# Performance work log

Hardware: AMD Instinct MI355X
Metric: run time of the kernel (lower is better)

The kernel has to match this reference:

```python
import jax, jax.numpy as jnp
import numpy as np

DIM = 128
LAYERS = 3
N_NODES = 50000
N_EDGES = 640000
LN_EPS = 1e-5


def setup_inputs() -> dict:
    key = jax.random.key(0)
    ks = jax.random.split(key, 10)
    s = 1.0 / np.sqrt(DIM)
    x = jax.random.normal(ks[0], (N_NODES, DIM), dtype=jnp.float32)
    edge_index = jax.random.randint(ks[1], (2, N_EDGES), 0, N_NODES, dtype=jnp.int64)
    in_w = jax.random.uniform(ks[2], (DIM, DIM), jnp.float32, -s, s)
    in_b = jax.random.uniform(ks[3], (DIM,), jnp.float32, -s, s)
    w1 = jax.random.uniform(ks[4], (LAYERS, DIM, DIM), jnp.float32, -s, s)
    b1 = jax.random.uniform(ks[5], (LAYERS, DIM), jnp.float32, -s, s)
    w2 = jax.random.uniform(ks[6], (LAYERS, DIM, DIM), jnp.float32, -s, s)
    b2 = jax.random.uniform(ks[7], (LAYERS, DIM), jnp.float32, -s, s)
    ln_g = jnp.ones((LAYERS, DIM), jnp.float32)
    ln_b = jnp.zeros((LAYERS, DIM), jnp.float32)
    return {"x": x, "edge_index": edge_index, "in_w": in_w, "in_b": in_b,
            "w1": w1, "b1": b1, "w2": w2, "b2": b2, "ln_g": ln_g, "ln_b": ln_b}


def _layer_norm(z, g, b):
    mu = jnp.mean(z, axis=-1, keepdims=True)
    var = jnp.mean(jnp.square(z - mu), axis=-1, keepdims=True)
    return (z - mu) * jax.lax.rsqrt(var + LN_EPS) * g + b


def reference(x, edge_index, in_w, in_b, w1, b1, w2, b2, ln_g, ln_b):
    src, dst = edge_index[0], edge_index[1]
    n = x.shape[0]
    # degree is identical every layer in the original; compute once (same math)
    deg = jax.ops.segment_sum(jnp.ones(dst.shape, x.dtype), dst, num_segments=n)
    deg = jnp.maximum(deg, 1.0)[:, None]  # [N,1]
    h = x @ in_w + in_b  # [N,D]
    for i in range(w1.shape[0]):
        m = jax.ops.segment_sum(h[src], dst, num_segments=n) / deg  # gather+scatter
        mlp = jax.nn.relu(m @ w1[i] + b1[i]) @ w2[i] + b2[i]
        h = _layer_norm(h + mlp, ln_g[i], ln_b[i])
    return h
```

## Files before the change

### kernel.cpp

```cpp
#include <hip/hip_runtime.h>
#include <hip/hip_fp8.h>

#define DIM 128
#define LN_EPS 1e-5f

typedef __attribute__((ext_vector_type(8))) short s16x8;
typedef __attribute__((ext_vector_type(4))) float f32x4;
typedef __attribute__((ext_vector_type(2))) float f32x2;
typedef __attribute__((ext_vector_type(4))) unsigned int u32x4;

__device__ __forceinline__ unsigned short f2bf(float f) {
    unsigned u = __float_as_uint(f);
    unsigned r = u + 0x7fffu + ((u >> 16) & 1u);
    return (unsigned short)(r >> 16);
}
__device__ __forceinline__ float bf2f(unsigned short b) {
    return __uint_as_float(((unsigned)b) << 16);
}
__device__ __forceinline__ unsigned char f2fp8(float f) {
    return (unsigned char)__hip_cvt_float_to_fp8(f, __HIP_SATFINITE, __HIP_E4M3);
}
__device__ __forceinline__ void acc_fp8x4(float* a, unsigned v) {
    f32x2 lo = __builtin_amdgcn_cvt_pk_f32_fp8(v, false);
    f32x2 hi = __builtin_amdgcn_cvt_pk_f32_fp8(v, true);
    a[0] += lo[0]; a[1] += lo[1]; a[2] += hi[0]; a[3] += hi[1];
}
__device__ __forceinline__ void acc_fp8x16(float* a, u32x4 v) {
    acc_fp8x4(a + 0,  v[0]);
    acc_fp8x4(a + 4,  v[1]);
    acc_fp8x4(a + 8,  v[2]);
    acc_fp8x4(a + 12, v[3]);
}


__global__ __launch_bounds__(256) void prep(const float* __restrict__ in_w,
                                            const float* __restrict__ w1,
                                            const float* __restrict__ w2,
                                            unsigned short* __restrict__ wt, int L,
                                            const int* __restrict__ dst, int E,
                                            int* __restrict__ counts, int nWblk) {
    if ((int)blockIdx.x < nWblk) {
        int mat = blockIdx.x >> 3, part = blockIdx.x & 7;
        const float* src;
        if (mat == 0) src = in_w;
        else if (mat <= L) src = w1 + (size_t)(mat - 1) * DIM * DIM;
        else src = w2 + (size_t)(mat - 1 - L) * DIM * DIM;
        unsigned short* dstw = wt + (size_t)mat * DIM * DIM;
        int base = part * 2048 + threadIdx.x;
#pragma unroll
        for (int j = 0; j < 8; ++j) {
            int i = base + j * 256;
            int k = i >> 7, n = i & 127;
            dstw[n * DIM + k] = f2bf(src[i]);
        }
    } else {
        int b = blockIdx.x - nWblk;
        int i = (b * 256 + threadIdx.x) * 4;
        if (i + 3 < E) {
            int4 d = *(const int4*)(dst + i);
            atomicAdd(&counts[d.x], 1);
            atomicAdd(&counts[d.y], 1);
            atomicAdd(&counts[d.z], 1);
            atomicAdd(&counts[d.w], 1);
        } else {
            for (int j = i; j < E; ++j) atomicAdd(&counts[dst[j]], 1);
        }
    }
}


__global__ __launch_bounds__(256) void scan_all(const int* __restrict__ counts, int n,
                                                int* __restrict__ rowptr,
                                                int* __restrict__ cursor,
                                                float* __restrict__ dinv, int E) {
    __shared__ int wsum[4];
    int tid = threadIdx.x;
    int lane = tid & 63, wid = tid >> 6;

    int limit = blockIdx.x * 1024;
    int acc = 0;
    for (int i = tid * 4; i < limit; i += 1024) {
        int4 c4 = *(const int4*)(counts + i);
        acc += c4.x + c4.y + c4.z + c4.w;
    }
#pragma unroll
    for (int off = 32; off > 0; off >>= 1) acc += __shfl_xor(acc, off, 64);
    if (lane == 0) wsum[wid] = acc;
    __syncthreads();
    int bofs = wsum[0] + wsum[1] + wsum[2] + wsum[3];
    __syncthreads();

    if (blockIdx.x == 0 && tid == 0) rowptr[n] = E;

    int base = blockIdx.x * 1024 + tid * 4;
    int v[4];
#pragma unroll
    for (int j = 0; j < 4; ++j) {
        int i = base + j;
        v[j] = (i < n) ? counts[i] : 0;
    }
    int tsum = v[0] + v[1] + v[2] + v[3];
    int incl = tsum;
#pragma unroll
    for (int off = 1; off < 64; off <<= 1) {
        int t = __shfl_up(incl, off, 64);
        if (lane >= off) incl += t;
    }
    if (lane == 63) wsum[wid] = incl;
    __syncthreads();
    int wofs = 0;
    for (int w = 0; w < 4; ++w)
        if (w < wid) wofs += wsum[w];
    int excl = bofs + wofs + (incl - tsum);
#pragma unroll
    for (int j = 0; j < 4; ++j) {
        int i = base + j;
        if (i < n) {
            rowptr[i] = excl;
            cursor[i] = excl;
            dinv[i] = 1.0f / (float)((v[j] > 1) ? v[j] : 1);
            excl += v[j];
        }
    }
}


__global__ void fill_csr(const int* __restrict__ src, const int* __restrict__ dst, int E,
                         int* __restrict__ cursor, unsigned short* __restrict__ srcidx) {
    int i = (blockIdx.x * 256 + threadIdx.x) * 4;
    if (i + 3 < E) {
        int4 s4 = *(const int4*)(src + i);
        int4 d4 = *(const int4*)(dst + i);
        int p0 = atomicAdd(&cursor[d4.x], 1); srcidx[p0] = (unsigned short)s4.x;
        int p1 = atomicAdd(&cursor[d4.y], 1); srcidx[p1] = (unsigned short)s4.y;
        int p2 = atomicAdd(&cursor[d4.z], 1); srcidx[p2] = (unsigned short)s4.z;
        int p3 = atomicAdd(&cursor[d4.w], 1); srcidx[p3] = (unsigned short)s4.w;
    } else {
        for (int j = i; j < E; ++j) {
            int p = atomicAdd(&cursor[dst[j]], 1);
            srcidx[p] = (unsigned short)src[j];
        }
    }
}


__global__ __launch_bounds__(256) void gemm_bias32(const float* __restrict__ x,
                                                   const unsigned short* __restrict__ Wt,
                                                   const float* __restrict__ bias,
                                                   unsigned short* __restrict__ hb,
                                                   unsigned char* __restrict__ h8, int N) {
    __shared__ __align__(16) unsigned short X[32][136];
    __shared__ __align__(16) float Z[32][132];
    __shared__ __align__(16) float bias_s[128];

    int tid = threadIdx.x;
    int w = tid >> 6, lane = tid & 63;
    int quad = lane >> 4, l16 = lane & 15;
    int r0 = blockIdx.x * 32;
    int cs = w * 32;

    if (tid < 32) *(float4*)(bias_s + tid * 4) = *(const float4*)(bias + tid * 4);

    {
        int row = tid >> 3;
        int c0 = (tid & 7) * 16;
        int grow = r0 + row;
        u32x4 o0 = {0, 0, 0, 0}, o1 = {0, 0, 0, 0};
        if (grow < N) {
            const float4* xp = (const float4*)(x + ((size_t)grow << 7) + c0);
            float4 f0 = xp[0], f1 = xp[1], f2 = xp[2], f3 = xp[3];
            o0[0] = (unsigned)f2bf(f0.x) | ((unsigned)f2bf(f0.y) << 16);
            o0[1] = (unsigned)f2bf(f0.z) | ((unsigned)f2bf(f0.w) << 16);
            o0[2] = (unsigned)f2bf(f1.x) | ((unsigned)f2bf(f1.y) << 16);
            o0[3] = (unsigned)f2bf(f1.z) | ((unsigned)f2bf(f1.w) << 16);
            o1[0] = (unsigned)f2bf(f2.x) | ((unsigned)f2bf(f2.y) << 16);
            o1[1] = (unsigned)f2bf(f2.z) | ((unsigned)f2bf(f2.w) << 16);
            o1[2] = (unsigned)f2bf(f3.x) | ((unsigned)f2bf(f3.y) << 16);
            o1[3] = (unsigned)f2bf(f3.z) | ((unsigned)f2bf(f3.w) << 16);
        }
        *(u32x4*)(&X[row][c0])     = o0;
        *(u32x4*)(&X[row][c0 + 8]) = o1;
    }
    __syncthreads();

    f32x4 ac[2][2];
    ac[0][0] = (f32x4){0.f, 0.f, 0.f, 0.f}; ac[0][1] = (f32x4){0.f, 0.f, 0.f, 0.f};
    ac[1][0] = (f32x4){0.f, 0.f, 0.f, 0.f}; ac[1][1] = (f32x4){0.f, 0.f, 0.f, 0.f};
#pragma unroll
    for (int k0 = 0; k0 < 128; k0 += 32) {
        s16x8 b0 = *(const s16x8*)(Wt + ((size_t)(cs + l16) << 7) + quad * 8 + k0);
        s16x8 b1 = *(const s16x8*)(Wt + ((size_t)(cs + 16 + l16) << 7) + quad * 8 + k0);
        s16x8 a0 = *(const s16x8*)(&X[l16][quad * 8 + k0]);
        s16x8 a1 = *(const s16x8*)(&X[16 + l16][quad * 8 + k0]);
        ac[0][0] = __builtin_amdgcn_mfma_f32_16x16x32_bf16(a0, b0, ac[0][0], 0, 0, 0);
        ac[0][1] = __builtin_amdgcn_mfma_f32_16x16x32_bf16(a0, b1, ac[0][1], 0, 0, 0);
        ac[1][0] = __builtin_amdgcn_mfma_f32_16x16x32_bf16(a1, b0, ac[1][0], 0, 0, 0);
        ac[1][1] = __builtin_amdgcn_mfma_f32_16x16x32_bf16(a1, b1, ac[1][1], 0, 0, 0);
    }

#pragma unroll
    for (int rt = 0; rt < 2; ++rt) {
#pragma unroll
        for (int c = 0; c < 2; ++c) {
            int col = cs + c * 16 + l16;
            float bv = bias_s[col];
#pragma unroll
            for (int reg = 0; reg < 4; ++reg) {
                Z[rt * 16 + quad * 4 + reg][col] = ac[rt][c][reg] + bv;
            }
        }
    }
    __syncthreads();

    {
        int row = tid >> 3;
        int c0 = (tid & 7) * 16;
        int grow = r0 + row;
        if (grow < N) {
            u32x4 ob0, ob1, o8;
#pragma unroll
            for (int j = 0; j < 4; ++j) {
                float v0 = Z[row][c0 + 2 * j];
                float v1 = Z[row][c0 + 2 * j + 1];
                float v2 = Z[row][c0 + 8 + 2 * j];
                float v3 = Z[row][c0 + 8 + 2 * j + 1];
                ob0[j] = (unsigned)f2bf(v0) | ((unsigned)f2bf(v1) << 16);
                ob1[j] = (unsigned)f2bf(v2) | ((unsigned)f2bf(v3) << 16);
                float w0 = Z[row][c0 + 4 * j], w1 = Z[row][c0 + 4 * j + 1];
                float w2 = Z[row][c0 + 4 * j + 2], w3 = Z[row][c0 + 4 * j + 3];
                o8[j] = (unsigned)f2fp8(w0) | ((unsigned)f2fp8(w1) << 8)
                      | ((unsigned)f2fp8(w2) << 16) | ((unsigned)f2fp8(w3) << 24);
            }
            *(u32x4*)(hb + ((size_t)grow << 7) + c0)     = ob0;
            *(u32x4*)(hb + ((size_t)grow << 7) + c0 + 8) = ob1;
            *(u32x4*)(h8 + ((size_t)grow << 7) + c0)     = o8;
        }
    }
}


__global__ __launch_bounds__(256) void aggregate(const unsigned char* __restrict__ h8in,
                                                 const int* __restrict__ rowptr,
                                                 const unsigned short* __restrict__ srcidx,
                                                 const float* __restrict__ dinv,
                                                 unsigned short* __restrict__ mout, int N) {
    int tid = threadIdx.x;
    int w = tid >> 6, lane = tid & 63;
    int g = lane >> 3, li = lane & 7;
    int nd = blockIdx.x * 32 + w * 8 + g;
    bool nv = nd < N;

    int e  = nv ? rowptr[nd] : 0;
    int ee = nv ? rowptr[nd + 1] : 0;
    float di = nv ? dinv[nd] : 0.f;

    const unsigned char* hsl = h8in + li * 16;

    float a[16];
#pragma unroll
    for (int j = 0; j < 16; ++j) a[j] = 0.f;

#define GIDX(jj) (((jj) < ee) ? (int)srcidx[(jj)] : -1)
    int jA = e;
    int iA0 = GIDX(jA + 0), iA1 = GIDX(jA + 1), iA2 = GIDX(jA + 2), iA3 = GIDX(jA + 3);
    u32x4 A0 = {0, 0, 0, 0}, A1 = {0, 0, 0, 0}, A2 = {0, 0, 0, 0}, A3 = {0, 0, 0, 0};
    if (iA0 >= 0) A0 = *(const u32x4*)(hsl + ((size_t)iA0 << 7));
    if (iA1 >= 0) A1 = *(const u32x4*)(hsl + ((size_t)iA1 << 7));
    if (iA2 >= 0) A2 = *(const u32x4*)(hsl + ((size_t)iA2 << 7));
    if (iA3 >= 0) A3 = *(const u32x4*)(hsl + ((size_t)iA3 << 7));
    int jB = jA + 4;
    int iB0 = GIDX(jB + 0), iB1 = GIDX(jB + 1), iB2 = GIDX(jB + 2), iB3 = GIDX(jB + 3);

    while (__any(jA < ee)) {
        u32x4 B0 = {0, 0, 0, 0}, B1v = {0, 0, 0, 0}, B2v = {0, 0, 0, 0}, B3 = {0, 0, 0, 0};
        if (iB0 >= 0) B0  = *(const u32x4*)(hsl + ((size_t)iB0 << 7));
        if (iB1 >= 0) B1v = *(const u32x4*)(hsl + ((size_t)iB1 << 7));
        if (iB2 >= 0) B2v = *(const u32x4*)(hsl + ((size_t)iB2 << 7));
        if (iB3 >= 0) B3  = *(const u32x4*)(hsl + ((size_t)iB3 << 7));
        int jC = jB + 4;
        int iC0 = GIDX(jC + 0), iC1 = GIDX(jC + 1), iC2 = GIDX(jC + 2), iC3 = GIDX(jC + 3);
        acc_fp8x16(a, A0);
        acc_fp8x16(a, A1);
        acc_fp8x16(a, A2);
        acc_fp8x16(a, A3);
        jA = jB; A0 = B0; A1 = B1v; A2 = B2v; A3 = B3;
        jB = jC; iB0 = iC0; iB1 = iC1; iB2 = iC2; iB3 = iC3;
    }
#undef GIDX

    if (nv) {
        u32x4 o0, o1;
#pragma unroll
        for (int j = 0; j < 4; ++j) {
            unsigned lo0 = f2bf(a[2 * j]     * di);
            unsigned hi0 = f2bf(a[2 * j + 1] * di);
            o0[j] = lo0 | (hi0 << 16);
            unsigned lo1 = f2bf(a[8 + 2 * j]     * di);
            unsigned hi1 = f2bf(a[8 + 2 * j + 1] * di);
            o1[j] = lo1 | (hi1 << 16);
        }
        unsigned short* mp = mout + ((size_t)nd << 7) + li * 16;
        *(u32x4*)(mp)     = o0;
        *(u32x4*)(mp + 8) = o1;
    }
}


__global__ __launch_bounds__(256) void mlp_ln(const unsigned short* __restrict__ hin,
                                              const unsigned short* __restrict__ m,
                                              const unsigned short* __restrict__ W1t,
                                              const float* __restrict__ B1,
                                              const unsigned short* __restrict__ W2t,
                                              const float* __restrict__ B2,
                                              const float* __restrict__ G,
                                              const float* __restrict__ Bb,
                                              unsigned short* __restrict__ hout,
                                              unsigned char* __restrict__ h8out,
                                              float* __restrict__ out_f32, int N) {
    __shared__ unsigned short M[32][132];
    __shared__ unsigned short P[32][132];
    __shared__ float s1p[4][32], s2p[4][32];

    int tid = threadIdx.x;
    int w = tid >> 6, lane = tid & 63;
    int quad = lane >> 4, l16 = lane & 15;
    int r0 = blockIdx.x * 32;
    int cs = w * 32;

#pragma unroll
    for (int cc = 0; cc < 2; ++cc) {
        int c = tid + cc * 256;
        int row = c >> 4, colc = (c & 15) * 8;
        int grow = r0 + row;
        u32x4 v = {0, 0, 0, 0};
        if (grow < N) v = *(const u32x4*)(m + ((size_t)grow << 7) + colc);
        *(u32x4*)(&M[row][colc]) = v;
    }
    __syncthreads();

    unsigned short hvr[2][2][4];
#pragma unroll
    for (int rt = 0; rt < 2; ++rt) {
#pragma unroll
        for (int c = 0; c < 2; ++c) {
            int col = cs + c * 16 + l16;
#pragma unroll
            for (int reg = 0; reg < 4; ++reg) {
                int grow = r0 + rt * 16 + quad * 4 + reg;
                hvr[rt][c][reg] = (grow < N) ? hin[((size_t)grow << 7) + col] : (unsigned short)0;
            }
        }
    }

    f32x4 ac1[2][2];
    ac1[0][0] = (f32x4){0.f, 0.f, 0.f, 0.f}; ac1[0][1] = (f32x4){0.f, 0.f, 0.f, 0.f};
    ac1[1][0] = (f32x4){0.f, 0.f, 0.f, 0.f}; ac1[1][1] = (f32x4){0.f, 0.f, 0.f, 0.f};
#pragma unroll
    for (int k0 = 0; k0 < 128; k0 += 32) {
        s16x8 b0 = *(const s16x8*)(W1t + ((size_t)(cs + l16) << 7) + quad * 8 + k0);
        s16x8 b1 = *(const s16x8*)(W1t + ((size_t)(cs + 16 + l16) << 7) + quad * 8 + k0);
        s16x8 a0 = *(const s16x8*)(&M[l16][quad * 8 + k0]);
        s16x8 a1 = *(const s16x8*)(&M[16 + l16][quad * 8 + k0]);
        ac1[0][0] = __builtin_amdgcn_mfma_f32_16x16x32_bf16(a0, b0, ac1[0][0], 0, 0, 0);
        ac1[0][1] = __builtin_amdgcn_mfma_f32_16x16x32_bf16(a0, b1, ac1[0][1], 0, 0, 0);
        ac1[1][0] = __builtin_amdgcn_mfma_f32_16x16x32_bf16(a1, b0, ac1[1][0], 0, 0, 0);
        ac1[1][1] = __builtin_amdgcn_mfma_f32_16x16x32_bf16(a1, b1, ac1[1][1], 0, 0, 0);
    }
#pragma unroll
    for (int rt = 0; rt < 2; ++rt) {
#pragma unroll
        for (int c = 0; c < 2; ++c) {
            int col = cs + c * 16 + l16;
            float bv = B1[col];
#pragma unroll
            for (int reg = 0; reg < 4; ++reg) {
                float v = fmaxf(ac1[rt][c][reg] + bv, 0.f);
                P[rt * 16 + quad * 4 + reg][col] = f2bf(v);
            }
        }
    }
    __syncthreads();

    f32x4 ac2[2][2];
    ac2[0][0] = (f32x4){0.f, 0.f, 0.f, 0.f}; ac2[0][1] = (f32x4){0.f, 0.f, 0.f, 0.f};
    ac2[1][0] = (f32x4){0.f, 0.f, 0.f, 0.f}; ac2[1][1] = (f32x4){0.f, 0.f, 0.f, 0.f};
#pragma unroll
    for (int k0 = 0; k0 < 128; k0 += 32) {
        s16x8 b0 = *(const s16x8*)(W2t + ((size_t)(cs + l16) << 7) + quad * 8 + k0);
        s16x8 b1 = *(const s16x8*)(W2t + ((size_t)(cs + 16 + l16) << 7) + quad * 8 + k0);
        s16x8 a0 = *(const s16x8*)(&P[l16][quad * 8 + k0]);
        s16x8 a1 = *(const s16x8*)(&P[16 + l16][quad * 8 + k0]);
        ac2[0][0] = __builtin_amdgcn_mfma_f32_16x16x32_bf16(a0, b0, ac2[0][0], 0, 0, 0);
        ac2[0][1] = __builtin_amdgcn_mfma_f32_16x16x32_bf16(a0, b1, ac2[0][1], 0, 0, 0);
        ac2[1][0] = __builtin_amdgcn_mfma_f32_16x16x32_bf16(a1, b0, ac2[1][0], 0, 0, 0);
        ac2[1][1] = __builtin_amdgcn_mfma_f32_16x16x32_bf16(a1, b1, ac2[1][1], 0, 0, 0);
    }

    float z[2][2][4];
    float ps1[2][4] = {{0, 0, 0, 0}, {0, 0, 0, 0}};
    float ps2[2][4] = {{0, 0, 0, 0}, {0, 0, 0, 0}};
#pragma unroll
    for (int rt = 0; rt < 2; ++rt) {
#pragma unroll
        for (int c = 0; c < 2; ++c) {
            int col = cs + c * 16 + l16;
            float b2v = B2[col];
#pragma unroll
            for (int reg = 0; reg < 4; ++reg) {
                float hv = bf2f(hvr[rt][c][reg]);
                float zz = ac2[rt][c][reg] + b2v + hv;
                z[rt][c][reg] = zz;
                ps1[rt][reg] += zz;
                ps2[rt][reg] += zz * zz;
            }
        }
    }
#pragma unroll
    for (int off = 1; off < 16; off <<= 1) {
#pragma unroll
        for (int rt = 0; rt < 2; ++rt) {
#pragma unroll
            for (int reg = 0; reg < 4; ++reg) {
                ps1[rt][reg] += __shfl_xor(ps1[rt][reg], off, 64);
                ps2[rt][reg] += __shfl_xor(ps2[rt][reg], off, 64);
            }
        }
    }
    if (l16 == 0) {
#pragma unroll
        for (int rt = 0; rt < 2; ++rt) {
#pragma unroll
            for (int reg = 0; reg < 4; ++reg) {
                s1p[w][rt * 16 + quad * 4 + reg] = ps1[rt][reg];
                s2p[w][rt * 16 + quad * 4 + reg] = ps2[rt][reg];
            }
        }
    }
    __syncthreads();

#pragma unroll
    for (int rt = 0; rt < 2; ++rt) {
#pragma unroll
        for (int reg = 0; reg < 4; ++reg) {
            int row = rt * 16 + quad * 4 + reg;
            float S1 = s1p[0][row] + s1p[1][row] + s1p[2][row] + s1p[3][row];
            float S2 = s2p[0][row] + s2p[1][row] + s2p[2][row] + s2p[3][row];
            float mean = S1 * (1.0f / 128.0f);
            float var = S2 * (1.0f / 128.0f) - mean * mean;
            float rs = rsqrtf(var + LN_EPS);
            int grow = r0 + row;
            if (grow < N) {
#pragma unroll
                for (int c = 0; c < 2; ++c) {
                    int col = cs + c * 16 + l16;
                    float o = (z[rt][c][reg] - mean) * rs * G[col] + Bb[col];
                    if (out_f32) {
                        out_f32[((size_t)grow << 7) + col] = o;
                    } else {
                        hout[((size_t)grow << 7) + col] = f2bf(o);
                        h8out[((size_t)grow << 7) + col] = f2fp8(o);
                    }
                }
            }
        }
    }
}


extern "C" void kernel_launch(void* const* d_in, const int* in_sizes, int n_in,
                              void* d_out, int out_size, void* d_ws, size_t ws_size,
                              hipStream_t stream) {
    const float* x    = (const float*)d_in[0];
    const int*   ei   = (const int*)d_in[1];
    const float* in_w = (const float*)d_in[2];
    const float* in_b = (const float*)d_in[3];
    const float* w1   = (const float*)d_in[4];
    const float* b1   = (const float*)d_in[5];
    const float* w2   = (const float*)d_in[6];
    const float* b2   = (const float*)d_in[7];
    const float* ln_g = (const float*)d_in[8];
    const float* ln_b = (const float*)d_in[9];

    const int N = in_sizes[0] / DIM;
    const int E = in_sizes[1] / 2;
    const int LAYERS = in_sizes[4] / (DIM * DIM);

    const int* e_src = ei;
    const int* e_dst = ei + E;

    char* ws = (char*)d_ws;
    unsigned short* hb0    = (unsigned short*)ws;  ws += (size_t)N * DIM * 2;
    unsigned short* hb1    = (unsigned short*)ws;  ws += (size_t)N * DIM * 2;
    unsigned char*  h8a    = (unsigned char*)ws;   ws += (size_t)N * DIM;
    unsigned char*  h8b    = (unsigned char*)ws;   ws += (size_t)N * DIM;
    int*            counts = (int*)ws;             ws += (size_t)N * 4;
    int*            rowptr = (int*)ws;             ws += (size_t)(N + 1) * 4;
    int*            cursor = (int*)ws;             ws += (size_t)N * 4;
    float*          dinv   = (float*)ws;           ws += (size_t)N * 4;
    unsigned short* srcidx = (unsigned short*)ws;  ws += (size_t)E * 2;
    unsigned short* wt     = (unsigned short*)ws;  ws += (size_t)(2 * LAYERS + 1) * DIM * DIM * 2;
    unsigned short* mbuf   = (unsigned short*)ws;  ws += (size_t)N * DIM * 2;

    const int nScanBlocks = (N + 1023) / 1024;
    const int nMat = 2 * LAYERS + 1;
    const int nWblk = nMat * 8;

    (void)hipMemsetAsync(counts, 0, (size_t)N * 4, stream);
    prep<<<nWblk + (E + 1023) / 1024, 256, 0, stream>>>(in_w, w1, w2, wt, LAYERS,
                                                        e_dst, E, counts, nWblk);
    scan_all<<<nScanBlocks, 256, 0, stream>>>(counts, N, rowptr, cursor, dinv, E);
    gemm_bias32<<<(N + 31) / 32, 256, 0, stream>>>(x, wt, in_b, hb0, h8a, N);
    fill_csr<<<(E + 1023) / 1024, 256, 0, stream>>>(e_src, e_dst, E, cursor, srcidx);

    const unsigned short* w1t = wt + (size_t)DIM * DIM;
    const unsigned short* w2t = wt + (size_t)(1 + LAYERS) * DIM * DIM;

    int tile_grid = (N + 31) / 32;
    unsigned short* hin  = hb0;  unsigned char* h8in  = h8a;
    unsigned short* hout = hb1;  unsigned char* h8out = h8b;
    for (int i = 0; i < LAYERS; ++i) {
        float* out = (i == LAYERS - 1) ? (float*)d_out : nullptr;
        aggregate<<<tile_grid, 256, 0, stream>>>(h8in, rowptr, srcidx, dinv, mbuf, N);
        mlp_ln<<<tile_grid, 256, 0, stream>>>(hin, mbuf,
                                              w1t + (size_t)i * DIM * DIM, b1 + (size_t)i * DIM,
                                              w2t + (size_t)i * DIM * DIM, b2 + (size_t)i * DIM,
                                              ln_g + (size_t)i * DIM, ln_b + (size_t)i * DIM,
                                              hout, h8out, out, N);
        unsigned short* t = hin; hin = hout; hout = t;
        unsigned char* t8 = h8in; h8in = h8out; h8out = t8;
    }
}
```

Before: 321.6 us.

## Restructure MLP+LayerNorm kernel so each wave owns 16 full rows

The fused MLP/LayerNorm kernel now gives each wave 16 complete rows across all 128 output columns, instead of splitting columns across waves over a shared 32-row tile. The A operand is read straight from global memory, the ReLU intermediate goes to a per-wave LDS slice, and LayerNorm statistics are reduced with shuffles only. This removes all block-level barriers and the cross-wave LDS reduction. In exchange each wave holds more accumulators (16 f32x4 tiles), raising register pressure, and the block tile grows to 64 rows, so the grid is halved.

```diff
diff --git a/kernel.cpp b/kernel.cpp
--- a/kernel.cpp
+++ b/kernel.cpp
@@ -317,149 +317,116 @@
                                               unsigned short* __restrict__ hout,
                                               unsigned char* __restrict__ h8out,
                                               float* __restrict__ out_f32, int N) {
-    __shared__ unsigned short M[32][132];
-    __shared__ unsigned short P[32][132];
-    __shared__ float s1p[4][32], s2p[4][32];
+    __shared__ __align__(16) unsigned short Pw[4][16][136];
 
     int tid = threadIdx.x;
     int w = tid >> 6, lane = tid & 63;
     int quad = lane >> 4, l16 = lane & 15;
-    int r0 = blockIdx.x * 32;
-    int cs = w * 32;
-
-#pragma unroll
-    for (int cc = 0; cc < 2; ++cc) {
-        int c = tid + cc * 256;
-        int row = c >> 4, colc = (c & 15) * 8;
-        int grow = r0 + row;
-        u32x4 v = {0, 0, 0, 0};
-        if (grow < N) v = *(const u32x4*)(m + ((size_t)grow << 7) + colc);
-        *(u32x4*)(&M[row][colc]) = v;
-    }
-    __syncthreads();
-
-    unsigned short hvr[2][2][4];
-#pragma unroll
-    for (int rt = 0; rt < 2; ++rt) {
-#pragma unroll
-        for (int c = 0; c < 2; ++c) {
-            int col = cs + c * 16 + l16;
+    int rw = blockIdx.x * 64 + w * 16;
+
+    f32x4 ac1[8];
+#pragma unroll
+    for (int t = 0; t < 8; ++t) ac1[t] = (f32x4){0.f, 0.f, 0.f, 0.f};
+    {
+        int arow = rw + l16;
+        bool av = arow < N;
+        const unsigned short* ap = m + ((size_t)(av ? arow : 0) << 7) + quad * 8;
+#pragma unroll
+        for (int ks = 0; ks < 4; ++ks) {
+            s16x8 a = {0, 0, 0, 0, 0, 0, 0, 0};
+            if (av) a = *(const s16x8*)(ap + ks * 32);
+#pragma unroll
+            for (int t = 0; t < 8; ++t) {
+                s16x8 b = *(const s16x8*)(W1t + ((size_t)(t * 16 + l16) << 7) + quad * 8 + ks * 32);
+                ac1[t] = __builtin_amdgcn_mfma_f32_16x16x32_bf16(a, b, ac1[t], 0, 0, 0);
+            }
+        }
+    }
+
+#pragma unroll
+    for (int t = 0; t < 8; ++t) {
+        float bv = B1[t * 16 + l16];
+#pragma unroll
+        for (int reg = 0; reg < 4; ++reg) {
+            float v = fmaxf(ac1[t][reg] + bv, 0.f);
+            Pw[w][quad * 4 + reg][t * 16 + l16] = f2bf(v);
+        }
+    }
+
+    f32x4 ac2[8];
+#pragma unroll
+    for (int t = 0; t < 8; ++t) ac2[t] = (f32x4){0.f, 0.f, 0.f, 0.f};
+#pragma unroll
+    for (int ks = 0; ks < 4; ++ks) {
+        s16x8 a = *(const s16x8*)(&Pw[w][l16][quad * 8 + ks * 32]);
+#pragma unroll
+        for (int t = 0; t < 8; ++t) {
+            s16x8 b = *(const s16x8*)(W2t + ((size_t)(t * 16 + l16) << 7) + quad * 8 + ks * 32);
+            ac2[t] = __builtin_amdgcn_mfma_f32_16x16x32_bf16(a, b, ac2[t], 0, 0, 0);
+        }
+    }
+
+    float b2v[8], gv[8], bbv[8];
+#pragma unroll
+    for (int t = 0; t < 8; ++t) {
+        b2v[t] = B2[t * 16 + l16];
+        gv[t]  = G[t * 16 + l16];
+        bbv[t] = Bb[t * 16 + l16];
+    }
+    unsigned short hvu[8][4];
+#pragma unroll
+    for (int reg = 0; reg < 4; ++reg) {
+        int gr = rw + quad * 4 + reg;
+        bool gvld = gr < N;
+        const unsigned short* hp = hin + ((size_t)(gvld ? gr : 0) << 7);
+#pragma unroll
+        for (int t = 0; t < 8; ++t) {
+            hvu[t][reg] = gvld ? hp[t * 16 + l16] : (unsigned short)0;
+        }
+    }
+
+    float ps1[4][4], ps2[4][4];
+#pragma unroll
+    for (int vw = 0; vw < 4; ++vw) {
+#pragma unroll
+        for (int reg = 0; reg < 4; ++reg) {
+            float z0 = ac2[2 * vw][reg] + b2v[2 * vw] + bf2f(hvu[2 * vw][reg]);
+            float z1 = ac2[2 * vw + 1][reg] + b2v[2 * vw + 1] + bf2f(hvu[2 * vw + 1][reg]);
+            ps1[vw][reg] = z0 + z1;
+            ps2[vw][reg] = z0 * z0 + z1 * z1;
+        }
+    }
+#pragma unroll
+    for (int off = 1; off < 16; off <<= 1) {
+#pragma unroll
+        for (int vw = 0; vw < 4; ++vw) {
 #pragma unroll
             for (int reg = 0; reg < 4; ++reg) {
-                int grow = r0 + rt * 16 + quad * 4 + reg;
-                hvr[rt][c][reg] = (grow < N) ? hin[((size_t)grow << 7) + col] : (unsigned short)0;
+                ps1[vw][reg] += __shfl_xor(ps1[vw][reg], off, 64);
+                ps2[vw][reg] += __shfl_xor(ps2[vw][reg], off, 64);
             }
         }
     }
 
-    f32x4 ac1[2][2];
-    ac1[0][0] = (f32x4){0.f, 0.f, 0.f, 0.f}; ac1[0][1] = (f32x4){0.f, 0.f, 0.f, 0.f};
-    ac1[1][0] = (f32x4){0.f, 0.f, 0.f, 0.f}; ac1[1][1] = (f32x4){0.f, 0.f, 0.f, 0.f};
-#pragma unroll
-    for (int k0 = 0; k0 < 128; k0 += 32) {
-        s16x8 b0 = *(const s16x8*)(W1t + ((size_t)(cs + l16) << 7) + quad * 8 + k0);
-        s16x8 b1 = *(const s16x8*)(W1t + ((size_t)(cs + 16 + l16) << 7) + quad * 8 + k0);
-        s16x8 a0 = *(const s16x8*)(&M[l16][quad * 8 + k0]);
-        s16x8 a1 = *(const s16x8*)(&M[16 + l16][quad * 8 + k0]);
-        ac1[0][0] = __builtin_amdgcn_mfma_f32_16x16x32_bf16(a0, b0, ac1[0][0], 0, 0, 0);
-        ac1[0][1] = __builtin_amdgcn_mfma_f32_16x16x32_bf16(a0, b1, ac1[0][1], 0, 0, 0);
-        ac1[1][0] = __builtin_amdgcn_mfma_f32_16x16x32_bf16(a1, b0, ac1[1][0], 0, 0, 0);
-        ac1[1][1] = __builtin_amdgcn_mfma_f32_16x16x32_bf16(a1, b1, ac1[1][1], 0, 0, 0);
-    }
-#pragma unroll
-    for (int rt = 0; rt < 2; ++rt) {
-#pragma unroll
-        for (int c = 0; c < 2; ++c) {
-            int col = cs + c * 16 + l16;
-            float bv = B1[col];
-#pragma unroll
-            for (int reg = 0; reg < 4; ++reg) {
-                float v = fmaxf(ac1[rt][c][reg] + bv, 0.f);
-                P[rt * 16 + quad * 4 + reg][col] = f2bf(v);
-            }
-        }
-    }
-    __syncthreads();
-
-    f32x4 ac2[2][2];
-    ac2[0][0] = (f32x4){0.f, 0.f, 0.f, 0.f}; ac2[0][1] = (f32x4){0.f, 0.f, 0.f, 0.f};
-    ac2[1][0] = (f32x4){0.f, 0.f, 0.f, 0.f}; ac2[1][1] = (f32x4){0.f, 0.f, 0.f, 0.f};
-#pragma unroll
-    for (int k0 = 0; k0 < 128; k0 += 32) {
-        s16x8 b0 = *(const s16x8*)(W2t + ((size_t)(cs + l16) << 7) + quad * 8 + k0);
-        s16x8 b1 = *(const s16x8*)(W2t + ((size_t)(cs + 16 + l16) << 7) + quad * 8 + k0);
-        s16x8 a0 = *(const s16x8*)(&P[l16][quad * 8 + k0]);
-        s16x8 a1 = *(const s16x8*)(&P[16 + l16][quad * 8 + k0]);
-        ac2[0][0] = __builtin_amdgcn_mfma_f32_16x16x32_bf16(a0, b0, ac2[0][0], 0, 0, 0);
-        ac2[0][1] = __builtin_amdgcn_mfma_f32_16x16x32_bf16(a0, b1, ac2[0][1], 0, 0, 0);
-        ac2[1][0] = __builtin_amdgcn_mfma_f32_16x16x32_bf16(a1, b0, ac2[1][0], 0, 0, 0);
-        ac2[1][1] = __builtin_amdgcn_mfma_f32_16x16x32_bf16(a1, b1, ac2[1][1], 0, 0, 0);
-    }
-
-    float z[2][2][4];
-    float ps1[2][4] = {{0, 0, 0, 0}, {0, 0, 0, 0}};
-    float ps2[2][4] = {{0, 0, 0, 0}, {0, 0, 0, 0}};
-#pragma unroll
-    for (int rt = 0; rt < 2; ++rt) {
-#pragma unroll
-        for (int c = 0; c < 2; ++c) {
-            int col = cs + c * 16 + l16;
-            float b2v = B2[col];
-#pragma unroll
-            for (int reg = 0; reg < 4; ++reg) {
-                float hv = bf2f(hvr[rt][c][reg]);
-                float zz = ac2[rt][c][reg] + b2v + hv;
-                z[rt][c][reg] = zz;
-                ps1[rt][reg] += zz;
-                ps2[rt][reg] += zz * zz;
-            }
-        }
-    }
-#pragma unroll
-    for (int off = 1; off < 16; off <<= 1) {
-#pragma unroll
-        for (int rt = 0; rt < 2; ++rt) {
-#pragma unroll
-            for (int reg = 0; reg < 4; ++reg) {
-                ps1[rt][reg] += __shfl_xor(ps1[rt][reg], off, 64);
-                ps2[rt][reg] += __shfl_xor(ps2[rt][reg], off, 64);
-            }
-        }
-    }
-    if (l16 == 0) {
-#pragma unroll
-        for (int rt = 0; rt < 2; ++rt) {
-#pragma unroll
-            for (int reg = 0; reg < 4; ++reg) {
-                s1p[w][rt * 16 + quad * 4 + reg] = ps1[rt][reg];
-                s2p[w][rt * 16 + quad * 4 + reg] = ps2[rt][reg];
-            }
-        }
-    }
-    __syncthreads();
-
-#pragma unroll
-    for (int rt = 0; rt < 2; ++rt) {
-#pragma unroll
-        for (int reg = 0; reg < 4; ++reg) {
-            int row = rt * 16 + quad * 4 + reg;
-            float S1 = s1p[0][row] + s1p[1][row] + s1p[2][row] + s1p[3][row];
-            float S2 = s2p[0][row] + s2p[1][row] + s2p[2][row] + s2p[3][row];
-            float mean = S1 * (1.0f / 128.0f);
-            float var = S2 * (1.0f / 128.0f) - mean * mean;
-            float rs = rsqrtf(var + LN_EPS);
-            int grow = r0 + row;
-            if (grow < N) {
-#pragma unroll
-                for (int c = 0; c < 2; ++c) {
-                    int col = cs + c * 16 + l16;
-                    float o = (z[rt][c][reg] - mean) * rs * G[col] + Bb[col];
-                    if (out_f32) {
-                        out_f32[((size_t)grow << 7) + col] = o;
-                    } else {
-                        hout[((size_t)grow << 7) + col] = f2bf(o);
-                        h8out[((size_t)grow << 7) + col] = f2fp8(o);
-                    }
+#pragma unroll
+    for (int reg = 0; reg < 4; ++reg) {
+        float S1 = ((ps1[0][reg] + ps1[1][reg]) + ps1[2][reg]) + ps1[3][reg];
+        float S2 = ((ps2[0][reg] + ps2[1][reg]) + ps2[2][reg]) + ps2[3][reg];
+        float mean = S1 * (1.0f / 128.0f);
+        float var = S2 * (1.0f / 128.0f) - mean * mean;
+        float rs = rsqrtf(var + LN_EPS);
+        int gr = rw + quad * 4 + reg;
+        if (gr < N) {
+#pragma unroll
+            for (int t = 0; t < 8; ++t) {
+                int col = t * 16 + l16;
+                float z = ac2[t][reg] + b2v[t] + bf2f(hvu[t][reg]);
+                float o = (z - mean) * rs * gv[t] + bbv[t];
+                if (out_f32) {
+                    out_f32[((size_t)gr << 7) + col] = o;
+                } else {
+                    hout[((size_t)gr << 7) + col] = f2bf(o);
+                    h8out[((size_t)gr << 7) + col] = f2fp8(o);
                 }
             }
         }
@@ -515,17 +482,18 @@
     const unsigned short* w1t = wt + (size_t)DIM * DIM;
     const unsigned short* w2t = wt + (size_t)(1 + LAYERS) * DIM * DIM;
 
-    int tile_grid = (N + 31) / 32;
+    int agg_grid = (N + 31) / 32;
+    int mlp_grid = (N + 63) / 64;
     unsigned short* hin  = hb0;  unsigned char* h8in  = h8a;
     unsigned short* hout = hb1;  unsigned char* h8out = h8b;
     for (int i = 0; i < LAYERS; ++i) {
         float* out = (i == LAYERS - 1) ? (float*)d_out : nullptr;
-        aggregate<<<tile_grid, 256, 0, stream>>>(h8in, rowptr, srcidx, dinv, mbuf, N);
-        mlp_ln<<<tile_grid, 256, 0, stream>>>(hin, mbuf,
-                                              w1t + (size_t)i * DIM * DIM, b1 + (size_t)i * DIM,
-                                              w2t + (size_t)i * DIM * DIM, b2 + (size_t)i * DIM,
-                                              ln_g + (size_t)i * DIM, ln_b + (size_t)i * DIM,
-                                              hout, h8out, out, N);
+        aggregate<<<agg_grid, 256, 0, stream>>>(h8in, rowptr, srcidx, dinv, mbuf, N);
+        mlp_ln<<<mlp_grid, 256, 0, stream>>>(hin, mbuf,
+                                             w1t + (size_t)i * DIM * DIM, b1 + (size_t)i * DIM,
+                                             w2t + (size_t)i * DIM * DIM, b2 + (size_t)i * DIM,
+                                             ln_g + (size_t)i * DIM, ln_b + (size_t)i * DIM,
+                                             hout, h8out, out, N);
         unsigned short* t = hin; hin = hout; hout = t;
         unsigned char* t8 = h8in; h8in = h8out; h8out = t8;
     }
```

New measurement: 391.9 us. +21.8%, slower.

## Fuse CSR fill into projection GEMM launch; load MLP A operand directly

Applied to the files above, without the earlier changes.

Merges the fill_csr kernel into the input-projection GEMM as extra blocks of a single launch, so the independent atomic CSR fill overlaps with the GEMM and one launch is saved. In mlp_ln, the aggregated-message tile is no longer staged through shared memory with a barrier. MFMA A fragments are instead read straight from global memory per lane. This removes an LDS round trip and a sync, but the fused kernel carries the GEMM's shared-memory footprint for the fill blocks, and the direct loads may be less coalesced.

```diff
diff --git a/kernel.cpp b/kernel.cpp
--- a/kernel.cpp
+++ b/kernel.cpp
@@ -125,35 +125,40 @@
 }
 
 
-__global__ void fill_csr(const int* __restrict__ src, const int* __restrict__ dst, int E,
-                         int* __restrict__ cursor, unsigned short* __restrict__ srcidx) {
-    int i = (blockIdx.x * 256 + threadIdx.x) * 4;
-    if (i + 3 < E) {
-        int4 s4 = *(const int4*)(src + i);
-        int4 d4 = *(const int4*)(dst + i);
-        int p0 = atomicAdd(&cursor[d4.x], 1); srcidx[p0] = (unsigned short)s4.x;
-        int p1 = atomicAdd(&cursor[d4.y], 1); srcidx[p1] = (unsigned short)s4.y;
-        int p2 = atomicAdd(&cursor[d4.z], 1); srcidx[p2] = (unsigned short)s4.z;
-        int p3 = atomicAdd(&cursor[d4.w], 1); srcidx[p3] = (unsigned short)s4.w;
-    } else {
-        for (int j = i; j < E; ++j) {
-            int p = atomicAdd(&cursor[dst[j]], 1);
-            srcidx[p] = (unsigned short)src[j];
-        }
-    }
-}
-
-
-__global__ __launch_bounds__(256) void gemm_bias32(const float* __restrict__ x,
-                                                   const unsigned short* __restrict__ Wt,
-                                                   const float* __restrict__ bias,
-                                                   unsigned short* __restrict__ hb,
-                                                   unsigned char* __restrict__ h8, int N) {
+__global__ __launch_bounds__(256) void proj_fill(const float* __restrict__ x,
+                                                 const unsigned short* __restrict__ Wt,
+                                                 const float* __restrict__ bias,
+                                                 unsigned short* __restrict__ hb,
+                                                 unsigned char* __restrict__ h8, int N,
+                                                 const int* __restrict__ src,
+                                                 const int* __restrict__ dst, int E,
+                                                 int* __restrict__ cursor,
+                                                 unsigned short* __restrict__ srcidx,
+                                                 int gemmBlocks) {
     __shared__ __align__(16) unsigned short X[32][136];
     __shared__ __align__(16) float Z[32][132];
     __shared__ __align__(16) float bias_s[128];
 
     int tid = threadIdx.x;
+    if ((int)blockIdx.x >= gemmBlocks) {
+        int b = blockIdx.x - gemmBlocks;
+        int i = (b * 256 + tid) * 4;
+        if (i + 3 < E) {
+            int4 s4 = *(const int4*)(src + i);
+            int4 d4 = *(const int4*)(dst + i);
+            int p0 = atomicAdd(&cursor[d4.x], 1); srcidx[p0] = (unsigned short)s4.x;
+            int p1 = atomicAdd(&cursor[d4.y], 1); srcidx[p1] = (unsigned short)s4.y;
+            int p2 = atomicAdd(&cursor[d4.z], 1); srcidx[p2] = (unsigned short)s4.z;
+            int p3 = atomicAdd(&cursor[d4.w], 1); srcidx[p3] = (unsigned short)s4.w;
+        } else {
+            for (int j = i; j < E; ++j) {
+                int p = atomicAdd(&cursor[dst[j]], 1);
+                srcidx[p] = (unsigned short)src[j];
+            }
+        }
+        return;
+    }
+
     int w = tid >> 6, lane = tid & 63;
     int quad = lane >> 4, l16 = lane & 15;
     int r0 = blockIdx.x * 32;
@@ -317,7 +322,6 @@
                                               unsigned short* __restrict__ hout,
                                               unsigned char* __restrict__ h8out,
                                               float* __restrict__ out_f32, int N) {
-    __shared__ unsigned short M[32][132];
     __shared__ unsigned short P[32][132];
     __shared__ float s1p[4][32], s2p[4][32];
 
@@ -327,17 +331,6 @@
     int r0 = blockIdx.x * 32;
     int cs = w * 32;
 
-#pragma unroll
-    for (int cc = 0; cc < 2; ++cc) {
-        int c = tid + cc * 256;
-        int row = c >> 4, colc = (c & 15) * 8;
-        int grow = r0 + row;
-        u32x4 v = {0, 0, 0, 0};
-        if (grow < N) v = *(const u32x4*)(m + ((size_t)grow << 7) + colc);
-        *(u32x4*)(&M[row][colc]) = v;
-    }
-    __syncthreads();
-
     unsigned short hvr[2][2][4];
 #pragma unroll
     for (int rt = 0; rt < 2; ++rt) {
@@ -352,6 +345,12 @@
         }
     }
 
+    int ar0 = r0 + l16;
+    int ar1 = r0 + 16 + l16;
+    bool av0 = ar0 < N, av1 = ar1 < N;
+    const unsigned short* ap0 = m + ((size_t)(av0 ? ar0 : 0) << 7) + quad * 8;
+    const unsigned short* ap1 = m + ((size_t)(av1 ? ar1 : 0) << 7) + quad * 8;
+
     f32x4 ac1[2][2];
     ac1[0][0] = (f32x4){0.f, 0.f, 0.f, 0.f}; ac1[0][1] = (f32x4){0.f, 0.f, 0.f, 0.f};
     ac1[1][0] = (f32x4){0.f, 0.f, 0.f, 0.f}; ac1[1][1] = (f32x4){0.f, 0.f, 0.f, 0.f};
@@ -359,8 +358,10 @@
     for (int k0 = 0; k0 < 128; k0 += 32) {
         s16x8 b0 = *(const s16x8*)(W1t + ((size_t)(cs + l16) << 7) + quad * 8 + k0);
         s16x8 b1 = *(const s16x8*)(W1t + ((size_t)(cs + 16 + l16) << 7) + quad * 8 + k0);
-        s16x8 a0 = *(const s16x8*)(&M[l16][quad * 8 + k0]);
-        s16x8 a1 = *(const s16x8*)(&M[16 + l16][quad * 8 + k0]);
+        s16x8 a0 = {0, 0, 0, 0, 0, 0, 0, 0};
+        s16x8 a1 = {0, 0, 0, 0, 0, 0, 0, 0};
+        if (av0) a0 = *(const s16x8*)(ap0 + k0);
+        if (av1) a1 = *(const s16x8*)(ap1 + k0);
         ac1[0][0] = __builtin_amdgcn_mfma_f32_16x16x32_bf16(a0, b0, ac1[0][0], 0, 0, 0);
         ac1[0][1] = __builtin_amdgcn_mfma_f32_16x16x32_bf16(a0, b1, ac1[0][1], 0, 0, 0);
         ac1[1][0] = __builtin_amdgcn_mfma_f32_16x16x32_bf16(a1, b0, ac1[1][0], 0, 0, 0);
@@ -504,13 +505,16 @@
     const int nScanBlocks = (N + 1023) / 1024;
     const int nMat = 2 * LAYERS + 1;
     const int nWblk = nMat * 8;
+    const int gemmBlocks = (N + 31) / 32;
+    const int fillBlocks = (E + 1023) / 1024;
 
     (void)hipMemsetAsync(counts, 0, (size_t)N * 4, stream);
     prep<<<nWblk + (E + 1023) / 1024, 256, 0, stream>>>(in_w, w1, w2, wt, LAYERS,
                                                         e_dst, E, counts, nWblk);
     scan_all<<<nScanBlocks, 256, 0, stream>>>(counts, N, rowptr, cursor, dinv, E);
-    gemm_bias32<<<(N + 31) / 32, 256, 0, stream>>>(x, wt, in_b, hb0, h8a, N);
-    fill_csr<<<(E + 1023) / 1024, 256, 0, stream>>>(e_src, e_dst, E, cursor, srcidx);
+    proj_fill<<<gemmBlocks + fillBlocks, 256, 0, stream>>>(x, wt, in_b, hb0, h8a, N,
+                                                           e_src, e_dst, E, cursor, srcidx,
+                                                           gemmBlocks);
 
     const unsigned short* w1t = wt + (size_t)DIM * DIM;
     const unsigned short* w2t = wt + (size_t)(1 + LAYERS) * DIM * DIM;
```

After: 331.3 us. +3.0%, slower.
